# Optimization experiments

Measured on AMD Instinct MI355X. Metric: run time of the kernel, lower is better.

## Reference

```python
import jax, jax.numpy as jnp
import numpy as np

B, L, C, H, FF = 4, 1024, 1024, 16, 4096
D = C // H  # head_dim = 64
SCALE = (D * 2.0) ** -0.5  # scale_factor = 2.0


def layer_norm(x, g, b, eps=1e-5):
    mu = jnp.mean(x, axis=-1, keepdims=True)
    var = jnp.var(x, axis=-1, keepdims=True)
    return (x - mu) * jax.lax.rsqrt(var + eps) * g + b


def setup_inputs() -> dict:
    key = jax.random.key(0)
    ks = jax.random.split(key, 12)
    s = 0.02
    inp = {
        'x': jax.random.normal(ks[0], (B, L, C), jnp.float32),
        'attn_bias': jax.random.normal(ks[1], (B, H, L, L), jnp.float32),
        'attention_mask': jnp.zeros((B, 1, L, L), jnp.float32),
        'Wq': jax.random.normal(ks[2], (C, C), jnp.float32) * s,
        'bq': jnp.zeros((C,), jnp.float32),
        'Wk': jax.random.normal(ks[3], (C, C), jnp.float32) * s,
        'bk': jnp.zeros((C,), jnp.float32),
        'Wv': jax.random.normal(ks[4], (C, C), jnp.float32) * s,
        'bv': jnp.zeros((C,), jnp.float32),
        'Wo': jax.random.normal(ks[5], (C, C), jnp.float32) * s,
        'bo': jnp.zeros((C,), jnp.float32),
        'c_attn': jnp.ones((H,), jnp.float32),
        'W1': jax.random.normal(ks[6], (FF, C), jnp.float32) * s,
        'b1': jnp.zeros((FF,), jnp.float32),
        'W2': jax.random.normal(ks[7], (C, FF), jnp.float32) * s,
        'b2': jnp.zeros((C,), jnp.float32),
        'attn_ln_g': jnp.ones((C,), jnp.float32),
        'attn_ln_b': jnp.zeros((C,), jnp.float32),
        'attn_mid_ln_g': jnp.ones((C,), jnp.float32),
        'attn_mid_ln_b': jnp.zeros((C,), jnp.float32),
        'ffn_ln_g': jnp.ones((C,), jnp.float32),
        'ffn_ln_b': jnp.zeros((C,), jnp.float32),
        'ffn_mid_ln_g': jnp.ones((FF,), jnp.float32),
        'ffn_mid_ln_b': jnp.zeros((FF,), jnp.float32),
    }
    return inp


def reference(x, attn_bias, attention_mask, Wq, bq, Wk, bk, Wv, bv, Wo, bo,
              c_attn, W1, b1, W2, b2, attn_ln_g, attn_ln_b,
              attn_mid_ln_g, attn_mid_ln_b, ffn_ln_g, ffn_ln_b,
              ffn_mid_ln_g, ffn_mid_ln_b):
    # ---- attention block (pre-norm, normformer) ----
    residual = x
    h = layer_norm(x, attn_ln_g, attn_ln_b)
    q = (h @ Wq.T + bq).reshape(B, L, H, D).transpose(0, 2, 1, 3)  # (B,H,L,D)
    k = (h @ Wk.T + bk).reshape(B, L, H, D).transpose(0, 2, 1, 3)
    v = (h @ Wv.T + bv).reshape(B, L, H, D).transpose(0, 2, 1, 3)
    # scores with bias (src_len == tgt_len, so the -src_len: slice is full) and mask
    scores = jnp.einsum('bhld,bhsd->bhls', q, k) * SCALE + attn_bias + attention_mask
    w = jax.nn.softmax(scores, axis=-1)
    attn = jnp.einsum('bhls,bhsd->bhld', w, v)
    attn = attn * c_attn[None, :, None, None]  # per-head scale (scale_heads)
    attn = attn.transpose(0, 2, 1, 3).reshape(B, L, C)
    attn = attn @ Wo.T + bo
    attn = layer_norm(attn, attn_mid_ln_g, attn_mid_ln_b)  # normformer mid-LN
    x = residual + attn
    # ---- FFN block (pre-norm, normformer) ----
    residual = x
    h = layer_norm(x, ffn_ln_g, ffn_ln_b)
    h = jax.nn.gelu(h @ W1.T + b1, approximate=False)
    h = layer_norm(h, ffn_mid_ln_g, ffn_mid_ln_b)  # normformer mid-LN on d_ff
    h = h @ W2.T + b2
    x = residual + h
    return x
```

## Files before the change

### kernel.cpp

```cpp
#include <hip/hip_runtime.h>
#include <hip/hip_bf16.h>
#include <math.h>

#define BB 4
#define LL 1024
#define CC 1024
#define HH 16
#define DD 64
#define FFD 4096
#define MM (BB*LL)
#define ATT_SCALE 0.08838834764831845f

typedef __bf16 bf16x8 __attribute__((ext_vector_type(8)));
typedef float f32x4 __attribute__((ext_vector_type(4)));

#define F32_PATTERN 0x3F800000u

__device__ __forceinline__ float b2f(unsigned short u) {
  union { unsigned int i; float f; } v; v.i = ((unsigned int)u) << 16; return v.f;
}
__device__ __forceinline__ unsigned short f2b(float f) {
  union { float f; unsigned int i; } v; v.f = f;
  unsigned int x = v.i;
  return (unsigned short)((x + 0x7fffu + ((x >> 16) & 1u)) >> 16);
}
__device__ __forceinline__ float ld1(const void* p, size_t i, bool isf32) {
  return isf32 ? reinterpret_cast<const float*>(p)[i]
               : b2f(reinterpret_cast<const unsigned short*>(p)[i]);
}
__device__ __forceinline__ float4 ld4(const void* p, size_t i, bool isf32) {
  float4 r;
  if (isf32) {
    r = *reinterpret_cast<const float4*>(reinterpret_cast<const float*>(p) + i);
  } else {
    ushort4 u = *reinterpret_cast<const ushort4*>(reinterpret_cast<const unsigned short*>(p) + i);
    r.x = b2f(u.x); r.y = b2f(u.y); r.z = b2f(u.z); r.w = b2f(u.w);
  }
  return r;
}
__device__ __forceinline__ float wave_sum(float v) {
#pragma unroll
  for (int o = 32; o > 0; o >>= 1) v += __shfl_down(v, o, 64);
  return v;
}

typedef __attribute__((address_space(1))) const void* as1cv;
typedef __attribute__((address_space(3))) void* as3v;
__device__ __forceinline__ void glds16(const void* g, void* l) {
  __builtin_amdgcn_global_load_lds((as1cv)g, (as3v)l, 16, 0, 0);
}

template <int COLS>
__global__ __launch_bounds__(256) void k_ln(
    const void* __restrict__ src, int srcext,
    const void* __restrict__ g, const void* __restrict__ bta,
    const void* __restrict__ res,
    unsigned short* __restrict__ dst,
    const unsigned int* __restrict__ probe)
{
  const bool isf32 = (*probe == F32_PATTERN);
  const bool sf = srcext && isf32;
  constexpr int NCH = COLS / 1024;
  const int row = blockIdx.x;
  const int t = threadIdx.x;
  const size_t base = (size_t)row * COLS;
  float fv[NCH * 4];
  float s = 0.f, s2 = 0.f;
#pragma unroll
  for (int c = 0; c < NCH; ++c) {
    float4 u = ld4(src, base + (size_t)(t + 256 * c) * 4, sf);
    fv[c * 4 + 0] = u.x; fv[c * 4 + 1] = u.y; fv[c * 4 + 2] = u.z; fv[c * 4 + 3] = u.w;
    s += u.x + u.y + u.z + u.w;
    s2 += u.x * u.x + u.y * u.y + u.z * u.z + u.w * u.w;
  }
  s = wave_sum(s); s2 = wave_sum(s2);
  __shared__ float red1[4], red2[4], stats[2];
  const int wv = t >> 6;
  if ((t & 63) == 0) { red1[wv] = s; red2[wv] = s2; }
  __syncthreads();
  if (t == 0) {
    float S = red1[0] + red1[1] + red1[2] + red1[3];
    float S2 = red2[0] + red2[1] + red2[2] + red2[3];
    float mu = S / COLS;
    float var = S2 / COLS - mu * mu;
    stats[0] = mu; stats[1] = rsqrtf(fmaxf(var, 0.f) + 1e-5f);
  }
  __syncthreads();
  const float mu = stats[0], rsg = stats[1];
#pragma unroll
  for (int c = 0; c < NCH; ++c) {
    const int off = (t + 256 * c) * 4;
    float4 gv = ld4(g, off, isf32);
    float4 bv = ld4(bta, off, isf32);
    float r0 = 0.f, r1 = 0.f, r2 = 0.f, r3 = 0.f;
    if (res) {
      float4 rv = ld4(res, base + off, isf32);
      r0 = rv.x; r1 = rv.y; r2 = rv.z; r3 = rv.w;
    }
    ushort4 o;
    o.x = f2b((fv[c * 4 + 0] - mu) * rsg * gv.x + bv.x + r0);
    o.y = f2b((fv[c * 4 + 1] - mu) * rsg * gv.y + bv.y + r1);
    o.z = f2b((fv[c * 4 + 2] - mu) * rsg * gv.z + bv.z + r2);
    o.w = f2b((fv[c * 4 + 3] - mu) * rsg * gv.w + bv.w + r3);
    *reinterpret_cast<ushort4*>(&dst[base + off]) = o;
  }
}

__global__ __launch_bounds__(256) void k_w2b(
    const void* __restrict__ Wq, const void* __restrict__ Wk,
    const void* __restrict__ Wv, const void* __restrict__ Wo,
    const void* __restrict__ W1, const void* __restrict__ W2,
    unsigned short* __restrict__ dst, const unsigned int* __restrict__ probe)
{
  const bool isf32 = (*probe == F32_PATTERN);
  const size_t NW = (size_t)CC * CC;
  const size_t i = ((size_t)blockIdx.x * 256 + threadIdx.x) * 8;
  const void* src; size_t off;
  if      (i <     NW) { src = Wq; off = i; }
  else if (i < 2 * NW) { src = Wk; off = i - NW; }
  else if (i < 3 * NW) { src = Wv; off = i - 2 * NW; }
  else if (i < 4 * NW) { src = Wo; off = i - 3 * NW; }
  else if (i < 8 * NW) { src = W1; off = i - 4 * NW; }
  else                 { src = W2; off = i - 8 * NW; }
  ushort4 lo, hi;
  if (isf32) {
    const float* f = reinterpret_cast<const float*>(src) + off;
    float4 u = *reinterpret_cast<const float4*>(f);
    float4 v = *reinterpret_cast<const float4*>(f + 4);
    lo.x = f2b(u.x); lo.y = f2b(u.y); lo.z = f2b(u.z); lo.w = f2b(u.w);
    hi.x = f2b(v.x); hi.y = f2b(v.y); hi.z = f2b(v.z); hi.w = f2b(v.w);
  } else {
    const unsigned short* u = reinterpret_cast<const unsigned short*>(src) + off;
    lo = *reinterpret_cast<const ushort4*>(u);
    hi = *reinterpret_cast<const ushort4*>(u + 4);
  }
  *reinterpret_cast<ushort4*>(&dst[i])     = lo;
  *reinterpret_cast<ushort4*>(&dst[i + 4]) = hi;
}

template <int EPI>
__device__ __forceinline__ void gemm_core(
    const unsigned short* __restrict__ A,
    const unsigned short* __restrict__ W,
    const void* __restrict__ bias,
    const unsigned short* __restrict__ res,
    void* __restrict__ out, int outext,
    int M, int N, int K, bool isf32)
{
  __shared__ __align__(16) unsigned short As[128][32];
  __shared__ __align__(16) unsigned short Bs[128][32];
  const int t = threadIdx.x;
  const int wv = t >> 6, lane = t & 63;
  const int fr = lane & 15, kq = (lane >> 4) * 8;
  const int gx = gridDim.x;
  const int nwg = gx * gridDim.y;
  int lin = blockIdx.y * gx + blockIdx.x;
  if ((nwg & 7) == 0) lin = (lin & 7) * (nwg >> 3) + (lin >> 3);
  const int m0 = (lin / gx) * 128, n0 = (lin % gx) * 128;
  const int wr = (wv >> 1) * 64, wc = (wv & 1) * 64;

  f32x4 acc[4][4];
#pragma unroll
  for (int i = 0; i < 4; ++i)
#pragma unroll
    for (int j = 0; j < 4; ++j) acc[i][j] = (f32x4){0.f, 0.f, 0.f, 0.f};

  const int sr = t >> 2, sc = (t & 3) * 8;
  const unsigned short* ga = &A[(size_t)(m0 + sr) * K + sc];
  const unsigned short* gb = &W[(size_t)(n0 + sr) * K + sc];
  unsigned short* la = &As[0][0] + t * 8;
  unsigned short* lb = &Bs[0][0] + t * 8;
  const size_t rstep = (size_t)64 * K;

  for (int k0 = 0; k0 < K; k0 += 32) {
    __syncthreads();
    glds16(ga + k0, la);
    glds16(ga + rstep + k0, la + 2048);
    glds16(gb + k0, lb);
    glds16(gb + rstep + k0, lb + 2048);
    __syncthreads();
    bf16x8 af[4], wf[4];
#pragma unroll
    for (int mi = 0; mi < 4; ++mi)
      af[mi] = *reinterpret_cast<const bf16x8*>(&As[wr + mi * 16 + fr][kq]);
#pragma unroll
    for (int ni = 0; ni < 4; ++ni)
      wf[ni] = *reinterpret_cast<const bf16x8*>(&Bs[wc + ni * 16 + fr][kq]);
#pragma unroll
    for (int mi = 0; mi < 4; ++mi)
#pragma unroll
      for (int ni = 0; ni < 4; ++ni)
        acc[mi][ni] = __builtin_amdgcn_mfma_f32_16x16x32_bf16(af[mi], wf[ni], acc[mi][ni], 0, 0, 0);
  }

  const int q4 = (lane >> 4) * 4;
#pragma unroll
  for (int ni = 0; ni < 4; ++ni) {
    const int n = n0 + wc + ni * 16 + fr;
    const float bv = ld1(bias, n, isf32);
#pragma unroll
    for (int mi = 0; mi < 4; ++mi) {
#pragma unroll
      for (int r = 0; r < 4; ++r) {
        const int m = m0 + wr + mi * 16 + q4 + r;
        float vv = acc[mi][ni][r] + bv;
        if (EPI == 1) vv = 0.5f * vv * (1.f + erff(vv * 0.70710678118654752f));
        if (EPI == 2) vv += b2f(res[(size_t)m * N + n]);
        const size_t oi = (size_t)m * N + n;
        if (outext && isf32) reinterpret_cast<float*>(out)[oi] = vv;
        else                 reinterpret_cast<unsigned short*>(out)[oi] = f2b(vv);
      }
    }
  }
}

template <int EPI>
__global__ __launch_bounds__(256) void k_gemm(
    const unsigned short* __restrict__ A,
    const unsigned short* __restrict__ W,
    const void* __restrict__ bias,
    const unsigned short* __restrict__ res,
    void* __restrict__ out, int outext,
    int M, int N, int K,
    const unsigned int* __restrict__ probe)
{
  const bool isf32 = (*probe == F32_PATTERN);
  gemm_core<EPI>(A, W, bias, res, out, outext, M, N, K, isf32);
}

__global__ __launch_bounds__(256) void k_gemm_qkv(
    const unsigned short* __restrict__ A,
    const unsigned short* __restrict__ Wqb, const unsigned short* __restrict__ Wkb,
    const unsigned short* __restrict__ Wvb,
    const void* __restrict__ bq, const void* __restrict__ bk, const void* __restrict__ bv,
    unsigned short* __restrict__ oq, unsigned short* __restrict__ ok,
    unsigned short* __restrict__ ov,
    const unsigned int* __restrict__ probe)
{
  const bool isf32 = (*probe == F32_PATTERN);
  const int z = blockIdx.z;
  const unsigned short* W = (z == 0) ? Wqb : (z == 1) ? Wkb : Wvb;
  const void* bias = (z == 0) ? bq : (z == 1) ? bk : bv;
  unsigned short* out = (z == 0) ? oq : (z == 1) ? ok : ov;
  gemm_core<0>(A, W, bias, nullptr, out, 0, MM, CC, CC, isf32);
}

__global__ __launch_bounds__(256) void k_attn(
    const unsigned short* __restrict__ Q,
    const unsigned short* __restrict__ K,
    const unsigned short* __restrict__ V,
    const void* __restrict__ bias,
    const void* __restrict__ mask,
    const void* __restrict__ c_attn,
    unsigned short* __restrict__ ctx,
    const unsigned int* __restrict__ probe)
{
  const bool isf32 = (*probe == F32_PATTERN);
  const int qt = blockIdx.x, h = blockIdx.y, b = blockIdx.z;
  const int q0 = qt * 64;
  const int t = threadIdx.x;
  const int wv = t >> 6, lane = t & 63;
  const int a = lane & 15, quad = lane >> 4;

  __shared__ __align__(16) unsigned short Qs[64][72];
  __shared__ __align__(16) unsigned short Ks[64][72];
  __shared__ __align__(16) unsigned short Ps[64][72];
  __shared__ __align__(16) unsigned short Vt[64 * 66];

  {
    const int r = t >> 2, c0 = (t & 3) * 16;
    const unsigned short* qp = &Q[((size_t)(b * LL + q0 + r)) * CC + h * DD + c0];
    *reinterpret_cast<int4*>(&Qs[r][c0])     = *reinterpret_cast<const int4*>(qp);
    *reinterpret_cast<int4*>(&Qs[r][c0 + 8]) = *reinterpret_cast<const int4*>(qp + 8);
  }

  f32x4 Sacc[4], Oacc[4];
  float m_old[4] = {-1e30f, -1e30f, -1e30f, -1e30f};
  float l_run[4] = {0.f, 0.f, 0.f, 0.f};
#pragma unroll
  for (int i = 0; i < 4; ++i) Oacc[i] = (f32x4){0.f, 0.f, 0.f, 0.f};

  const int vd = t & 63, vs0 = (t >> 6) * 16;
  const int kr = t >> 2, kc0 = (t & 3) * 16;
  const int qrow_lane = wv * 16 + quad * 4;
  const size_t bias_row0 = ((size_t)(b * HH + h) * LL + q0) * LL;
  const size_t mask_row0 = ((size_t)(b * LL + q0)) * LL;

  for (int scn = 0; scn < 16; ++scn) {
    const int s0 = scn * 64;
    const unsigned short* kp = &K[((size_t)(b * LL + s0 + kr)) * CC + h * DD + kc0];
    const int4 kv0 = *reinterpret_cast<const int4*>(kp);
    const int4 kv1 = *reinterpret_cast<const int4*>(kp + 8);
    const unsigned short* vp = &V[((size_t)(b * LL + s0 + vs0)) * CC + h * DD + vd];
    unsigned short vvb[16];
#pragma unroll
    for (int j = 0; j < 16; ++j) vvb[j] = vp[(size_t)j * CC];
    float bm[16];
#pragma unroll
    for (int r = 0; r < 4; ++r) {
      const size_t br = bias_row0 + (size_t)(qrow_lane + r) * LL + s0 + a;
      const size_t mr = mask_row0 + (size_t)(qrow_lane + r) * LL + s0 + a;
#pragma unroll
      for (int nt = 0; nt < 4; ++nt)
        bm[r * 4 + nt] = ld1(bias, br + nt * 16, isf32) + ld1(mask, mr + nt * 16, isf32);
    }
    __syncthreads();
    *reinterpret_cast<int4*>(&Ks[kr][kc0])     = kv0;
    *reinterpret_cast<int4*>(&Ks[kr][kc0 + 8]) = kv1;
#pragma unroll
    for (int j = 0; j < 8; ++j) {
      ushort2 p; p.x = vvb[2 * j]; p.y = vvb[2 * j + 1];
      *reinterpret_cast<ushort2*>(&Vt[vd * 66 + vs0 + 2 * j]) = p;
    }
    __syncthreads();
#pragma unroll
    for (int nt = 0; nt < 4; ++nt) Sacc[nt] = (f32x4){0.f, 0.f, 0.f, 0.f};
#pragma unroll
    for (int ks = 0; ks < 2; ++ks) {
      bf16x8 af = *reinterpret_cast<const bf16x8*>(&Qs[wv * 16 + a][ks * 32 + quad * 8]);
#pragma unroll
      for (int nt = 0; nt < 4; ++nt) {
        bf16x8 bf = *reinterpret_cast<const bf16x8*>(&Ks[nt * 16 + a][ks * 32 + quad * 8]);
        Sacc[nt] = __builtin_amdgcn_mfma_f32_16x16x32_bf16(af, bf, Sacc[nt], 0, 0, 0);
      }
    }
#pragma unroll
    for (int r = 0; r < 4; ++r)
#pragma unroll
      for (int nt = 0; nt < 4; ++nt)
        Sacc[nt][r] = Sacc[nt][r] * ATT_SCALE + bm[r * 4 + nt];
#pragma unroll
    for (int r = 0; r < 4; ++r) {
      float mc = fmaxf(fmaxf(Sacc[0][r], Sacc[1][r]), fmaxf(Sacc[2][r], Sacc[3][r]));
      mc = fmaxf(mc, __shfl_xor(mc, 1, 64));
      mc = fmaxf(mc, __shfl_xor(mc, 2, 64));
      mc = fmaxf(mc, __shfl_xor(mc, 4, 64));
      mc = fmaxf(mc, __shfl_xor(mc, 8, 64));
      const float mn = fmaxf(m_old[r], mc);
      const float al = __expf(m_old[r] - mn);
      m_old[r] = mn;
      float ps = 0.f;
#pragma unroll
      for (int nt = 0; nt < 4; ++nt) {
        const float p = __expf(Sacc[nt][r] - mn);
        Sacc[nt][r] = p;
        ps += p;
      }
      ps += __shfl_xor(ps, 1, 64);
      ps += __shfl_xor(ps, 2, 64);
      ps += __shfl_xor(ps, 4, 64);
      ps += __shfl_xor(ps, 8, 64);
      l_run[r] = l_run[r] * al + ps;
#pragma unroll
      for (int dt = 0; dt < 4; ++dt) Oacc[dt][r] *= al;
    }
#pragma unroll
    for (int r = 0; r < 4; ++r)
#pragma unroll
      for (int nt = 0; nt < 4; ++nt)
        Ps[qrow_lane + r][nt * 16 + a] = f2b(Sacc[nt][r]);
    __syncthreads();
#pragma unroll
    for (int ks = 0; ks < 2; ++ks) {
      bf16x8 pf = *reinterpret_cast<const bf16x8*>(&Ps[wv * 16 + a][ks * 32 + quad * 8]);
#pragma unroll
      for (int dt = 0; dt < 4; ++dt) {
        union { ushort2 u2[4]; bf16x8 v; } u;
        const unsigned short* vp2 = &Vt[(dt * 16 + a) * 66 + ks * 32 + quad * 8];
        u.u2[0] = *reinterpret_cast<const ushort2*>(vp2);
        u.u2[1] = *reinterpret_cast<const ushort2*>(vp2 + 2);
        u.u2[2] = *reinterpret_cast<const ushort2*>(vp2 + 4);
        u.u2[3] = *reinterpret_cast<const ushort2*>(vp2 + 6);
        Oacc[dt] = __builtin_amdgcn_mfma_f32_16x16x32_bf16(pf, u.v, Oacc[dt], 0, 0, 0);
      }
    }
  }
  const float cah = ld1(c_attn, h, isf32);
#pragma unroll
  for (int r = 0; r < 4; ++r) {
    const float inv = cah / fmaxf(l_run[r], 1e-30f);
    unsigned short* op = &ctx[((size_t)(b * LL + q0 + qrow_lane + r)) * CC + h * DD + a];
#pragma unroll
    for (int dt = 0; dt < 4; ++dt)
      op[dt * 16] = f2b(Oacc[dt][r] * inv);
  }
}

extern "C" void kernel_launch(void* const* d_in, const int* in_sizes, int n_in,
                              void* d_out, int out_size, void* d_ws, size_t ws_size,
                              hipStream_t stream) {
  (void)in_sizes; (void)n_in; (void)out_size; (void)ws_size;
  const void* x    = d_in[0];
  const void* abia = d_in[1];
  const void* amsk = d_in[2];
  const void* Wq   = d_in[3];
  const void* bq   = d_in[4];
  const void* Wk   = d_in[5];
  const void* bk   = d_in[6];
  const void* Wv   = d_in[7];
  const void* bv   = d_in[8];
  const void* Wo   = d_in[9];
  const void* bo   = d_in[10];
  const void* ca   = d_in[11];
  const void* W1   = d_in[12];
  const void* b1   = d_in[13];
  const void* W2   = d_in[14];
  const void* b2   = d_in[15];
  const void* alg  = d_in[16];
  const void* alb  = d_in[17];
  const void* amg  = d_in[18];
  const void* amb  = d_in[19];
  const void* flg  = d_in[20];
  const void* flb  = d_in[21];
  const void* fmg  = d_in[22];
  const void* fmb  = d_in[23];
  const unsigned int* probe = (const unsigned int*)alg;

  unsigned short* S0 = (unsigned short*)d_ws;
  unsigned short* S1 = S0 + (size_t)MM * CC;
  unsigned short* S2 = S1 + (size_t)MM * CC;
  unsigned short* S3 = S2 + (size_t)MM * CC;
  unsigned short* S4 = S3 + (size_t)MM * CC;
  unsigned short* S5 = S4 + (size_t)MM * CC;
  unsigned short* WB = S5 + (size_t)MM * CC;
  unsigned short* Wqb = WB;
  unsigned short* Wkb = WB + (size_t)CC * CC;
  unsigned short* Wvb = WB + (size_t)2 * CC * CC;
  unsigned short* Wob = WB + (size_t)3 * CC * CC;
  unsigned short* W1b = WB + (size_t)4 * CC * CC;
  unsigned short* W2b = W1b + (size_t)FFD * CC;

  dim3 blk(256);
  dim3 g1(CC / 128, MM / 128);
  dim3 g2(FFD / 128, MM / 128);
  dim3 gqkv(CC / 128, MM / 128, 3);
  dim3 ga(LL / 64, HH, BB);

  k_w2b<<<6144, blk, 0, stream>>>(Wq, Wk, Wv, Wo, W1, W2, WB, probe);
  k_ln<CC><<<MM, blk, 0, stream>>>(x, 1, alg, alb, nullptr, S0, probe);
  k_gemm_qkv<<<gqkv, blk, 0, stream>>>(S0, Wqb, Wkb, Wvb, bq, bk, bv, S1, S2, S3, probe);
  k_attn<<<ga, blk, 0, stream>>>(S1, S2, S3, abia, amsk, ca, S4, probe);
  k_gemm<0><<<g1, blk, 0, stream>>>(S4, Wob, bo, nullptr, S5, 0, MM, CC, CC, probe);
  k_ln<CC><<<MM, blk, 0, stream>>>(S5, 0, amg, amb, x, S1, probe);
  k_ln<CC><<<MM, blk, 0, stream>>>(S1, 0, flg, flb, nullptr, S0, probe);
  k_gemm<1><<<g2, blk, 0, stream>>>(S0, W1b, b1, nullptr, S2, 0, MM, FFD, CC, probe);
  k_ln<FFD><<<MM, blk, 0, stream>>>(S2, 0, fmg, fmb, nullptr, S2, probe);
  k_gemm<2><<<g1, blk, 0, stream>>>(S2, W2b, b2, S1, d_out, 1, MM, CC, FFD, probe);
}
```

Before: 812.4 us.

## Use 64-wide N tiles for C-output GEMMs and 128-query attention tiles

GEMM core is templated on N-tile width, and the Wo and W2 GEMMs (N=1024) switch to 128x64 tiles. This doubles their workgroup count so more CUs have work, at the cost of less operand reuse per tile. Attention now processes 128 query rows per workgroup with 512 threads. Each K/V chunk loaded into shared memory is reused across twice as many queries, but there are half as many workgroups and each uses more LDS.

```diff
diff --git a/kernel.cpp b/kernel.cpp
--- a/kernel.cpp
+++ b/kernel.cpp
@@ -138,7 +138,7 @@
   *reinterpret_cast<ushort4*>(&dst[i + 4]) = hi;
 }
 
-template <int EPI>
+template <int EPI, int NT>
 __device__ __forceinline__ void gemm_core(
     const unsigned short* __restrict__ A,
     const unsigned short* __restrict__ W,
@@ -147,8 +147,9 @@
     void* __restrict__ out, int outext,
     int M, int N, int K, bool isf32)
 {
+  constexpr int BN = NT * 32;
   __shared__ __align__(16) unsigned short As[128][32];
-  __shared__ __align__(16) unsigned short Bs[128][32];
+  __shared__ __align__(16) unsigned short Bs[BN][32];
   const int t = threadIdx.x;
   const int wv = t >> 6, lane = t & 63;
   const int fr = lane & 15, kq = (lane >> 4) * 8;
@@ -156,14 +157,14 @@
   const int nwg = gx * gridDim.y;
   int lin = blockIdx.y * gx + blockIdx.x;
   if ((nwg & 7) == 0) lin = (lin & 7) * (nwg >> 3) + (lin >> 3);
-  const int m0 = (lin / gx) * 128, n0 = (lin % gx) * 128;
-  const int wr = (wv >> 1) * 64, wc = (wv & 1) * 64;
-
-  f32x4 acc[4][4];
+  const int m0 = (lin / gx) * 128, n0 = (lin % gx) * BN;
+  const int wr = (wv >> 1) * 64, wc = (wv & 1) * (BN / 2);
+
+  f32x4 acc[4][NT];
 #pragma unroll
   for (int i = 0; i < 4; ++i)
 #pragma unroll
-    for (int j = 0; j < 4; ++j) acc[i][j] = (f32x4){0.f, 0.f, 0.f, 0.f};
+    for (int j = 0; j < NT; ++j) acc[i][j] = (f32x4){0.f, 0.f, 0.f, 0.f};
 
   const int sr = t >> 2, sc = (t & 3) * 8;
   const unsigned short* ga = &A[(size_t)(m0 + sr) * K + sc];
@@ -177,25 +178,25 @@
     glds16(ga + k0, la);
     glds16(ga + rstep + k0, la + 2048);
     glds16(gb + k0, lb);
-    glds16(gb + rstep + k0, lb + 2048);
+    if (NT == 4) glds16(gb + rstep + k0, lb + 2048);
     __syncthreads();
-    bf16x8 af[4], wf[4];
+    bf16x8 af[4], wf[NT];
 #pragma unroll
     for (int mi = 0; mi < 4; ++mi)
       af[mi] = *reinterpret_cast<const bf16x8*>(&As[wr + mi * 16 + fr][kq]);
 #pragma unroll
-    for (int ni = 0; ni < 4; ++ni)
+    for (int ni = 0; ni < NT; ++ni)
       wf[ni] = *reinterpret_cast<const bf16x8*>(&Bs[wc + ni * 16 + fr][kq]);
 #pragma unroll
     for (int mi = 0; mi < 4; ++mi)
 #pragma unroll
-      for (int ni = 0; ni < 4; ++ni)
+      for (int ni = 0; ni < NT; ++ni)
         acc[mi][ni] = __builtin_amdgcn_mfma_f32_16x16x32_bf16(af[mi], wf[ni], acc[mi][ni], 0, 0, 0);
   }
 
   const int q4 = (lane >> 4) * 4;
 #pragma unroll
-  for (int ni = 0; ni < 4; ++ni) {
+  for (int ni = 0; ni < NT; ++ni) {
     const int n = n0 + wc + ni * 16 + fr;
     const float bv = ld1(bias, n, isf32);
 #pragma unroll
@@ -214,7 +215,7 @@
   }
 }
 
-template <int EPI>
+template <int EPI, int NT>
 __global__ __launch_bounds__(256) void k_gemm(
     const unsigned short* __restrict__ A,
     const unsigned short* __restrict__ W,
@@ -225,7 +226,7 @@
     const unsigned int* __restrict__ probe)
 {
   const bool isf32 = (*probe == F32_PATTERN);
-  gemm_core<EPI>(A, W, bias, res, out, outext, M, N, K, isf32);
+  gemm_core<EPI, NT>(A, W, bias, res, out, outext, M, N, K, isf32);
 }
 
 __global__ __launch_bounds__(256) void k_gemm_qkv(
@@ -242,10 +243,10 @@
   const unsigned short* W = (z == 0) ? Wqb : (z == 1) ? Wkb : Wvb;
   const void* bias = (z == 0) ? bq : (z == 1) ? bk : bv;
   unsigned short* out = (z == 0) ? oq : (z == 1) ? ok : ov;
-  gemm_core<0>(A, W, bias, nullptr, out, 0, MM, CC, CC, isf32);
-}
-
-__global__ __launch_bounds__(256) void k_attn(
+  gemm_core<0, 4>(A, W, bias, nullptr, out, 0, MM, CC, CC, isf32);
+}
+
+__global__ __launch_bounds__(512) void k_attn(
     const unsigned short* __restrict__ Q,
     const unsigned short* __restrict__ K,
     const unsigned short* __restrict__ V,
@@ -257,14 +258,14 @@
 {
   const bool isf32 = (*probe == F32_PATTERN);
   const int qt = blockIdx.x, h = blockIdx.y, b = blockIdx.z;
-  const int q0 = qt * 64;
+  const int q0 = qt * 128;
   const int t = threadIdx.x;
   const int wv = t >> 6, lane = t & 63;
   const int a = lane & 15, quad = lane >> 4;
 
-  __shared__ __align__(16) unsigned short Qs[64][72];
+  __shared__ __align__(16) unsigned short Qs[128][72];
   __shared__ __align__(16) unsigned short Ks[64][72];
-  __shared__ __align__(16) unsigned short Ps[64][72];
+  __shared__ __align__(16) unsigned short Ps[128][72];
   __shared__ __align__(16) unsigned short Vt[64 * 66];
 
   {
@@ -280,8 +281,8 @@
 #pragma unroll
   for (int i = 0; i < 4; ++i) Oacc[i] = (f32x4){0.f, 0.f, 0.f, 0.f};
 
-  const int vd = t & 63, vs0 = (t >> 6) * 16;
-  const int kr = t >> 2, kc0 = (t & 3) * 16;
+  const int vd = t & 63, vs0 = (t >> 6) * 8;
+  const int kr = t >> 3, kc0 = (t & 7) * 8;
   const int qrow_lane = wv * 16 + quad * 4;
   const size_t bias_row0 = ((size_t)(b * HH + h) * LL + q0) * LL;
   const size_t mask_row0 = ((size_t)(b * LL + q0)) * LL;
@@ -290,11 +291,10 @@
     const int s0 = scn * 64;
     const unsigned short* kp = &K[((size_t)(b * LL + s0 + kr)) * CC + h * DD + kc0];
     const int4 kv0 = *reinterpret_cast<const int4*>(kp);
-    const int4 kv1 = *reinterpret_cast<const int4*>(kp + 8);
     const unsigned short* vp = &V[((size_t)(b * LL + s0 + vs0)) * CC + h * DD + vd];
-    unsigned short vvb[16];
-#pragma unroll
-    for (int j = 0; j < 16; ++j) vvb[j] = vp[(size_t)j * CC];
+    unsigned short vvb[8];
+#pragma unroll
+    for (int j = 0; j < 8; ++j) vvb[j] = vp[(size_t)j * CC];
     float bm[16];
 #pragma unroll
     for (int r = 0; r < 4; ++r) {
@@ -305,10 +305,9 @@
         bm[r * 4 + nt] = ld1(bias, br + nt * 16, isf32) + ld1(mask, mr + nt * 16, isf32);
     }
     __syncthreads();
-    *reinterpret_cast<int4*>(&Ks[kr][kc0])     = kv0;
-    *reinterpret_cast<int4*>(&Ks[kr][kc0 + 8]) = kv1;
-#pragma unroll
-    for (int j = 0; j < 8; ++j) {
+    *reinterpret_cast<int4*>(&Ks[kr][kc0]) = kv0;
+#pragma unroll
+    for (int j = 0; j < 4; ++j) {
       ushort2 p; p.x = vvb[2 * j]; p.y = vvb[2 * j + 1];
       *reinterpret_cast<ushort2*>(&Vt[vd * 66 + vs0 + 2 * j]) = p;
     }
@@ -431,19 +430,20 @@
   unsigned short* W2b = W1b + (size_t)FFD * CC;
 
   dim3 blk(256);
-  dim3 g1(CC / 128, MM / 128);
+  dim3 blkA(512);
+  dim3 g1n(CC / 64, MM / 128);
   dim3 g2(FFD / 128, MM / 128);
   dim3 gqkv(CC / 128, MM / 128, 3);
-  dim3 ga(LL / 64, HH, BB);
+  dim3 ga(LL / 128, HH, BB);
 
   k_w2b<<<6144, blk, 0, stream>>>(Wq, Wk, Wv, Wo, W1, W2, WB, probe);
   k_ln<CC><<<MM, blk, 0, stream>>>(x, 1, alg, alb, nullptr, S0, probe);
   k_gemm_qkv<<<gqkv, blk, 0, stream>>>(S0, Wqb, Wkb, Wvb, bq, bk, bv, S1, S2, S3, probe);
-  k_attn<<<ga, blk, 0, stream>>>(S1, S2, S3, abia, amsk, ca, S4, probe);
-  k_gemm<0><<<g1, blk, 0, stream>>>(S4, Wob, bo, nullptr, S5, 0, MM, CC, CC, probe);
+  k_attn<<<ga, blkA, 0, stream>>>(S1, S2, S3, abia, amsk, ca, S4, probe);
+  k_gemm<0, 2><<<g1n, blk, 0, stream>>>(S4, Wob, bo, nullptr, S5, 0, MM, CC, CC, probe);
   k_ln<CC><<<MM, blk, 0, stream>>>(S5, 0, amg, amb, x, S1, probe);
   k_ln<CC><<<MM, blk, 0, stream>>>(S1, 0, flg, flb, nullptr, S0, probe);
-  k_gemm<1><<<g2, blk, 0, stream>>>(S0, W1b, b1, nullptr, S2, 0, MM, FFD, CC, probe);
+  k_gemm<1, 4><<<g2, blk, 0, stream>>>(S0, W1b, b1, nullptr, S2, 0, MM, FFD, CC, probe);
   k_ln<FFD><<<MM, blk, 0, stream>>>(S2, 0, fmg, fmb, nullptr, S2, probe);
-  k_gemm<2><<<g1, blk, 0, stream>>>(S2, W2b, b2, S1, d_out, 1, MM, CC, FFD, probe);
-}
+  k_gemm<2, 2><<<g1n, blk, 0, stream>>>(S2, W2b, b2, S1, d_out, 1, MM, CC, FFD, probe);
+}
```

Measured after the change: 789.5 us. 2.8% less time.
